# Optimization experiments

Hardware: AMD Instinct MI355X
Metric: run time of the kernel (lower is better)

## Reference

```python
import jax, jax.numpy as jnp
import numpy as np

B, T, DIM = 4, 4096, 1024
HEADS, DIM_HEAD = 16, 64
INNER = HEADS * DIM_HEAD
SCALE = DIM_HEAD ** -0.5


def setup_inputs() -> dict:
    key = jax.random.key(0)
    k1, k2, k3, k4 = jax.random.split(key, 4)
    x = jax.random.normal(k1, (B, T, DIM), dtype=jnp.float32)
    mask = jax.random.bernoulli(k2, 0.2, (B, T))  # True = padding
    W_qkv = jax.random.normal(k3, (DIM, 3 * INNER), dtype=jnp.float32) * (DIM ** -0.5)
    W_out = jax.random.normal(k4, (INNER, DIM), dtype=jnp.float32) * (INNER ** -0.5)
    b_out = jnp.zeros((DIM,), dtype=jnp.float32)
    return {"x": x, "mask": mask, "W_qkv": W_qkv, "W_out": W_out, "b_out": b_out}


def reference(x, mask, W_qkv, W_out, b_out):
    Bs, Ts, _ = x.shape
    qkv = x @ W_qkv                                       # [B,T,3*inner]
    q, k, v = jnp.split(qkv, 3, axis=-1)
    # [B,T,H,Dh] -> [B,H,T,Dh]
    reshape = lambda t: t.reshape(Bs, Ts, HEADS, DIM_HEAD).transpose(0, 2, 1, 3)
    q, k, v = reshape(q), reshape(k), reshape(v)
    q = q * SCALE
    k = jax.nn.softmax(k, axis=-2)                        # softmax over sequence dim
    # zero out padded positions AFTER softmax (faithful to original)
    k = jnp.where(mask[:, None, :, None], 0.0, k)
    context = jnp.einsum('bhnd,bhne->bhde', k, v)         # [B,H,Dh,Dh]
    out = jnp.einsum('bhnd,bhde->bhne', q, context)       # [B,H,T,Dh]
    out = out.transpose(0, 2, 1, 3).reshape(Bs, Ts, INNER)
    return out @ W_out + b_out                            # dropout: eval mode (identity)
```

## Files before the change

kernel.cpp:

```cpp
#include <hip/hip_runtime.h>
#include <math.h>


typedef __bf16 bf16;
typedef __attribute__((ext_vector_type(4))) float f32x4;
typedef __attribute__((ext_vector_type(8))) __bf16 bf16x8;
typedef __attribute__((ext_vector_type(4))) __bf16 bf16x4;

#define SCALE_ 0.125f

__device__ __forceinline__ void g2l16(const void* g, void* l) {
  __builtin_amdgcn_global_load_lds((const __attribute__((address_space(1))) void*)g,
                                   (__attribute__((address_space(3))) void*)l, 16, 0, 0);
}

__global__ __launch_bounds__(256) void k_cvt(const float* __restrict__ in,
                                             bf16* __restrict__ out, int n4) {
  int i = blockIdx.x * 256 + threadIdx.x;
  if (i >= n4) return;
  f32x4 v = ((const f32x4*)in)[i];
  bf16x4 o;
  o[0] = (bf16)v[0]; o[1] = (bf16)v[1]; o[2] = (bf16)v[2]; o[3] = (bf16)v[3];
  ((bf16x4*)out)[i] = o;
}

__global__ __launch_bounds__(256) void k_trans(const float* __restrict__ W,
                                               bf16* __restrict__ Wt) {
  __shared__ float t[32][33];
  int n0 = blockIdx.x * 32, k0 = blockIdx.y * 32;
  int tx = threadIdx.x & 31, ty = threadIdx.x >> 5;
  #pragma unroll
  for (int s = 0; s < 4; s++) {
    int k = ty + s * 8;
    t[k][tx] = W[(size_t)(k0 + k) * 3072 + 1024 + n0 + tx];
  }
  __syncthreads();
  #pragma unroll
  for (int s = 0; s < 4; s++) {
    int n = ty + s * 8;
    Wt[(size_t)(n0 + n) * 1024 + k0 + tx] = (bf16)t[tx][n];
  }
}

__global__ __launch_bounds__(256) void k_wq(const float* __restrict__ W,
                                            bf16* __restrict__ wqs) {
  int idx = blockIdx.x * 256 + threadIdx.x;
  int i = idx >> 8, d4 = idx & 255;
  f32x4 v = *(const f32x4*)(W + (size_t)i * 3072 + d4 * 4);
  bf16x4 o;
  o[0] = (bf16)(v[0] * SCALE_); o[1] = (bf16)(v[1] * SCALE_);
  o[2] = (bf16)(v[2] * SCALE_); o[3] = (bf16)(v[3] * SCALE_);
  *(bf16x4*)(wqs + (size_t)i * 1024 + d4 * 4) = o;
}

__global__ __launch_bounds__(256) void k_gemm1(const bf16* __restrict__ A,
                                               const bf16* __restrict__ Bt,
                                               bf16* __restrict__ kv) {
  __shared__ __align__(16) bf16 As[128 * 32];
  __shared__ __align__(16) bf16 Bs[128 * 32];
  const int tid = threadIdx.x;
  const int wave = tid >> 6, lane = tid & 63, l16 = lane & 15, quad = lane >> 4;
  const int wm = (wave >> 1) << 6, wn = (wave & 1) << 6;
  const int f = blockIdx.x, xcd = f & 7, w = f >> 3;
  const int row0 = (xcd * 16 + (w >> 4)) << 7;
  const int col0 = (w & 15) << 7;
  f32x4 acc[4][4] = {};
  for (int kt = 0; kt < 1024; kt += 32) {
    #pragma unroll
    for (int it = 0; it < 2; ++it) {
      const int cb = (wave * 2 + it) * 64;
      const int c = cb + lane;
      const int m = c >> 2, k8 = (c & 3) * 8;
      g2l16(A  + (size_t)(row0 + m) * 1024 + kt + k8, As + cb * 8);
      g2l16(Bt + (size_t)(col0 + m) * 1024 + kt + k8, Bs + cb * 8);
    }
    __syncthreads();
    bf16x8 af[4], bfr[4];
    #pragma unroll
    for (int i = 0; i < 4; i++) af[i]  = *(const bf16x8*)(As + (wm + i * 16 + l16) * 32 + quad * 8);
    #pragma unroll
    for (int j = 0; j < 4; j++) bfr[j] = *(const bf16x8*)(Bs + (wn + j * 16 + l16) * 32 + quad * 8);
    #pragma unroll
    for (int i = 0; i < 4; i++)
      #pragma unroll
      for (int j = 0; j < 4; j++)
        acc[i][j] = __builtin_amdgcn_mfma_f32_16x16x32_bf16(af[i], bfr[j], acc[i][j], 0, 0, 0);
    __syncthreads();
  }
  #pragma unroll
  for (int i = 0; i < 4; i++) {
    const int gm0 = row0 + wm + i * 16 + quad * 4;
    #pragma unroll
    for (int j = 0; j < 4; j++) {
      const int gc = col0 + wn + j * 16 + l16;
      #pragma unroll
      for (int r = 0; r < 4; r++)
        kv[(size_t)(gm0 + r) * 2048 + gc] = (bf16)acc[i][j][r];
    }
  }
}

__global__ __launch_bounds__(256) void k_ctx(const bf16* __restrict__ kv,
                                             const int* __restrict__ mask,
                                             float* __restrict__ sumexp,
                                             float* __restrict__ ctx) {
  __shared__ float Lk[64][68];
  __shared__ float Lv[64][68];
  __shared__ float Sst[64][33];
  const int blk = blockIdx.x, tid = threadIdx.x;
  const int wave = tid >> 6, lane = tid & 63;
  const int ns = blk & 7, h = (blk >> 3) & 15, b = blk >> 7;
  const int d0 = (lane & 7) * 8, e0 = (lane >> 3) * 8;
  const int g = tid & 7;
  float acc[8][8] = {};
  float sum8[8] = {};
  const int nbase = ns * 512;
  for (int ch = 0; ch < 8; ++ch) {
    const int n0 = nbase + ch * 64;
    __syncthreads();
    #pragma unroll
    for (int it = 0; it < 2; ++it) {
      const int idx = it * 256 + tid;
      const int row = idx >> 3;
      const int gn = b * 4096 + n0 + row;
      const float m = mask[gn] ? 0.f : 1.f;
      bf16x8 t8 = *(const bf16x8*)(kv + (size_t)gn * 2048 + h * 64 + g * 8);
      float e[8];
      #pragma unroll
      for (int j = 0; j < 8; j++) { e[j] = __expf((float)t8[j]); sum8[j] += e[j]; }
      f32x4 lo, hi;
      lo[0] = e[0] * m; lo[1] = e[1] * m; lo[2] = e[2] * m; lo[3] = e[3] * m;
      hi[0] = e[4] * m; hi[1] = e[5] * m; hi[2] = e[6] * m; hi[3] = e[7] * m;
      *(f32x4*)&Lk[row][g * 8] = lo;
      *(f32x4*)&Lk[row][g * 8 + 4] = hi;
    }
    #pragma unroll
    for (int it = 0; it < 2; ++it) {
      const int idx = it * 256 + tid;
      const int row = idx >> 3;
      const int gn = b * 4096 + n0 + row;
      bf16x8 t8 = *(const bf16x8*)(kv + (size_t)gn * 2048 + 1024 + h * 64 + g * 8);
      f32x4 lo, hi;
      lo[0] = (float)t8[0]; lo[1] = (float)t8[1]; lo[2] = (float)t8[2]; lo[3] = (float)t8[3];
      hi[0] = (float)t8[4]; hi[1] = (float)t8[5]; hi[2] = (float)t8[6]; hi[3] = (float)t8[7];
      *(f32x4*)&Lv[row][g * 8] = lo;
      *(f32x4*)&Lv[row][g * 8 + 4] = hi;
    }
    __syncthreads();
    #pragma unroll 4
    for (int t = 0; t < 16; t++) {
      const int n = (wave << 4) + t;
      f32x4 ka = *(const f32x4*)&Lk[n][d0];
      f32x4 kb = *(const f32x4*)&Lk[n][d0 + 4];
      f32x4 va = *(const f32x4*)&Lv[n][e0];
      f32x4 vb = *(const f32x4*)&Lv[n][e0 + 4];
      float kk[8] = {ka[0], ka[1], ka[2], ka[3], kb[0], kb[1], kb[2], kb[3]};
      float vv[8] = {va[0], va[1], va[2], va[3], vb[0], vb[1], vb[2], vb[3]};
      #pragma unroll
      for (int a = 0; a < 8; a++)
        #pragma unroll
        for (int c = 0; c < 8; c++) acc[a][c] += kk[a] * vv[c];
    }
  }
  __syncthreads();
  float* r0 = &Lk[0][0];
  float* r1 = &Lv[0][0];
  if (wave < 2) {
    float* r = wave ? r1 : r0;
    #pragma unroll
    for (int a = 0; a < 8; a++)
      #pragma unroll
      for (int c = 0; c < 8; c++) r[(d0 + a) * 64 + e0 + c] = acc[a][c];
  }
  {
    const int rg = tid >> 3;
    #pragma unroll
    for (int j = 0; j < 8; j++) Sst[g * 8 + j][rg] = sum8[j];
  }
  __syncthreads();
  if (wave >= 2) {
    float* r = (wave == 3) ? r1 : r0;
    #pragma unroll
    for (int a = 0; a < 8; a++)
      #pragma unroll
      for (int c = 0; c < 8; c++) r[(d0 + a) * 64 + e0 + c] += acc[a][c];
  } else if (tid < 64) {
    float s = 0.f;
    #pragma unroll 8
    for (int rg = 0; rg < 32; rg++) s += Sst[tid][rg];
    atomicAdd(&sumexp[b * 1024 + h * 64 + tid], s);
  }
  __syncthreads();
  float* cbase = ctx + ((size_t)(b * 16 + h) << 12);
  for (int i = tid; i < 4096; i += 256) atomicAdd(cbase + i, r0[i] + r1[i]);
}

__global__ __launch_bounds__(256) void k_m2(const float* __restrict__ ctx,
                                            const float* __restrict__ sumexp,
                                            const float* __restrict__ Wout,
                                            bf16* __restrict__ M2t) {
  __shared__ float Lc[64][64];
  __shared__ float Linv[64];
  const int b = blockIdx.z, h = blockIdx.y, jt = blockIdx.x;
  const int tid = threadIdx.x, dg = tid >> 6, jl = tid & 63;
  const float* cbase = ctx + ((size_t)(b * 16 + h) << 12);
  for (int i = tid; i < 4096; i += 256) (&Lc[0][0])[i] = cbase[i];
  if (tid < 64) Linv[tid] = 1.f / sumexp[b * 1024 + h * 64 + tid];
  __syncthreads();
  float acc[4][16] = {};
  const int j0 = jt * 256 + jl;
  for (int e = 0; e < 64; e++) {
    const float* wrow = Wout + (size_t)(h * 64 + e) * 1024 + j0;
    float w0 = wrow[0], w1 = wrow[64], w2 = wrow[128], w3 = wrow[192];
    #pragma unroll
    for (int dd = 0; dd < 16; dd++) {
      float c = Lc[dg * 16 + dd][e];
      acc[0][dd] += c * w0; acc[1][dd] += c * w1;
      acc[2][dd] += c * w2; acc[3][dd] += c * w3;
    }
  }
  #pragma unroll
  for (int jj = 0; jj < 4; jj++) {
    const size_t jrow = ((size_t)b << 20) + (size_t)(jt * 256 + jl + jj * 64) * 1024 + h * 64 + dg * 16;
    #pragma unroll
    for (int dd = 0; dd < 16; dd++)
      M2t[jrow + dd] = (bf16)(acc[jj][dd] * Linv[dg * 16 + dd]);
  }
}

__global__ __launch_bounds__(256) void k_m3(const bf16* __restrict__ M2t,
                                            const bf16* __restrict__ wqs,
                                            bf16* __restrict__ M3t) {
  __shared__ __align__(16) bf16 As[128 * 32];
  __shared__ __align__(16) bf16 Bs[128 * 32];
  const int tid = threadIdx.x;
  const int wave = tid >> 6, lane = tid & 63, l16 = lane & 15, quad = lane >> 4;
  const int wm = (wave >> 1) << 6, wn = (wave & 1) << 6;
  const int row0 = blockIdx.y << 7, col0 = blockIdx.x << 7;
  const bf16* A  = M2t + ((size_t)blockIdx.z << 20);
  bf16*       C  = M3t + ((size_t)blockIdx.z << 20);
  f32x4 acc[4][4] = {};
  for (int kt = 0; kt < 1024; kt += 32) {
    #pragma unroll
    for (int it = 0; it < 2; ++it) {
      const int cb = (wave * 2 + it) * 64;
      const int c = cb + lane;
      const int m = c >> 2, k8 = (c & 3) * 8;
      g2l16(A   + (size_t)(row0 + m) * 1024 + kt + k8, As + cb * 8);
      g2l16(wqs + (size_t)(col0 + m) * 1024 + kt + k8, Bs + cb * 8);
    }
    __syncthreads();
    bf16x8 af[4], bfr[4];
    #pragma unroll
    for (int i = 0; i < 4; i++) af[i]  = *(const bf16x8*)(As + (wm + i * 16 + l16) * 32 + quad * 8);
    #pragma unroll
    for (int j = 0; j < 4; j++) bfr[j] = *(const bf16x8*)(Bs + (wn + j * 16 + l16) * 32 + quad * 8);
    #pragma unroll
    for (int i = 0; i < 4; i++)
      #pragma unroll
      for (int j = 0; j < 4; j++)
        acc[i][j] = __builtin_amdgcn_mfma_f32_16x16x32_bf16(af[i], bfr[j], acc[i][j], 0, 0, 0);
    __syncthreads();
  }
  #pragma unroll
  for (int i = 0; i < 4; i++) {
    const int gm0 = row0 + wm + i * 16 + quad * 4;
    #pragma unroll
    for (int j = 0; j < 4; j++) {
      const int gc = col0 + wn + j * 16 + l16;
      #pragma unroll
      for (int r = 0; r < 4; r++)
        C[(size_t)(gm0 + r) * 1024 + gc] = (bf16)acc[i][j][r];
    }
  }
}

__global__ __launch_bounds__(256) void k_gemm2(const bf16* __restrict__ A,
                                               const bf16* __restrict__ M3t,
                                               const float* __restrict__ bias,
                                               float* __restrict__ out) {
  __shared__ __align__(16) bf16 As[128 * 32];
  __shared__ __align__(16) bf16 Bs[128 * 32];
  const int tid = threadIdx.x;
  const int wave = tid >> 6, lane = tid & 63, l16 = lane & 15, quad = lane >> 4;
  const int wm = (wave >> 1) << 6, wn = (wave & 1) << 6;
  const int f = blockIdx.x, xcd = f & 7, w = f >> 3;
  const int row0 = (xcd * 16 + (w >> 3)) << 7;
  const int col0 = (w & 7) << 7;
  const bf16* Bt = M3t + ((size_t)(row0 >> 12) << 20);
  f32x4 acc[4][4] = {};
  for (int kt = 0; kt < 1024; kt += 32) {
    #pragma unroll
    for (int it = 0; it < 2; ++it) {
      const int cb = (wave * 2 + it) * 64;
      const int c = cb + lane;
      const int m = c >> 2, k8 = (c & 3) * 8;
      g2l16(A  + (size_t)(row0 + m) * 1024 + kt + k8, As + cb * 8);
      g2l16(Bt + (size_t)(col0 + m) * 1024 + kt + k8, Bs + cb * 8);
    }
    __syncthreads();
    bf16x8 af[4], bfr[4];
    #pragma unroll
    for (int i = 0; i < 4; i++) af[i]  = *(const bf16x8*)(As + (wm + i * 16 + l16) * 32 + quad * 8);
    #pragma unroll
    for (int j = 0; j < 4; j++) bfr[j] = *(const bf16x8*)(Bs + (wn + j * 16 + l16) * 32 + quad * 8);
    #pragma unroll
    for (int i = 0; i < 4; i++)
      #pragma unroll
      for (int j = 0; j < 4; j++)
        acc[i][j] = __builtin_amdgcn_mfma_f32_16x16x32_bf16(af[i], bfr[j], acc[i][j], 0, 0, 0);
    __syncthreads();
  }
  float bj[4];
  #pragma unroll
  for (int j = 0; j < 4; j++) bj[j] = bias[col0 + wn + j * 16 + l16];
  #pragma unroll
  for (int i = 0; i < 4; i++) {
    const int gm0 = row0 + wm + i * 16 + quad * 4;
    #pragma unroll
    for (int j = 0; j < 4; j++) {
      const int gc = col0 + wn + j * 16 + l16;
      #pragma unroll
      for (int r = 0; r < 4; r++)
        out[(size_t)(gm0 + r) * 1024 + gc] = acc[i][j][r] + bj[j];
    }
  }
}

extern "C" void kernel_launch(void* const* d_in, const int* in_sizes, int n_in,
                              void* d_out, int out_size, void* d_ws, size_t ws_size,
                              hipStream_t stream) {
  const float* x    = (const float*)d_in[0];
  const int*   mask = (const int*)d_in[1];
  const float* Wqkv = (const float*)d_in[2];
  const float* Wout = (const float*)d_in[3];
  const float* bout = (const float*)d_in[4];
  float* out = (float*)d_out;
  char* ws = (char*)d_ws;
  bf16*  xb     = (bf16*)(ws);
  bf16*  wt     = (bf16*)(ws + 33554432);
  bf16*  wqs    = (bf16*)(ws + 37748736);
  bf16*  kv     = (bf16*)(ws + 39845888);
  float* sumexp = (float*)(ws + 106954752);
  float* ctx    = (float*)(ws + 106971136);
  bf16*  m2t    = (bf16*)(ws + 108019712);
  bf16*  m3t    = (bf16*)(ws + 116408320);

  hipMemsetAsync(sumexp, 0, 16384 + 1048576, stream);
  k_cvt  <<<16384, 256, 0, stream>>>(x, xb, 4194304);
  k_trans<<<dim3(64, 32), 256, 0, stream>>>(Wqkv, wt);
  k_wq   <<<1024, 256, 0, stream>>>(Wqkv, wqs);
  k_gemm1<<<2048, 256, 0, stream>>>(xb, wt, kv);
  k_ctx  <<<512, 256, 0, stream>>>(kv, mask, sumexp, ctx);
  k_m2   <<<dim3(4, 16, 4), 256, 0, stream>>>(ctx, sumexp, Wout, m2t);
  k_m3   <<<dim3(8, 8, 4), 256, 0, stream>>>(m2t, wqs, m3t);
  k_gemm2<<<1024, 256, 0, stream>>>(xb, m3t, bout, out);
}
```

Baseline: 350.9 us.

## Triple-buffer GEMM K-loop with async LDS prefetch and XOR-swizzled tiles

Replaces the synchronous load-then-compute K loop in the three bf16 MFMA GEMMs with a three-stage LDS ring buffer. Tiles are prefetched two steps ahead through global_load_lds, and vmcnt waits plus raw barriers let global loads overlap MFMA work. An XOR swizzle on the 8-element k-chunks is meant to cut LDS bank conflicts on fragment reads. In exchange, LDS use per block triples and the code depends on hand-counted vmcnt values that must match the number of outstanding loads.

Result: slower. 363.1 us (+3.5%).

```diff
diff --git a/kernel.cpp b/kernel.cpp
--- a/kernel.cpp
+++ b/kernel.cpp
@@ -53,11 +53,67 @@
   *(bf16x4*)(wqs + (size_t)i * 1024 + d4 * 4) = o;
 }
 
+__device__ __forceinline__ void stage_tile(const bf16* __restrict__ A,
+                                           const bf16* __restrict__ Bt,
+                                           int row0, int col0, int kt,
+                                           bf16* as, bf16* bs,
+                                           int wave, int lane) {
+  #pragma unroll
+  for (int it = 0; it < 2; ++it) {
+    const int cb = (wave * 2 + it) * 64;
+    const int c = cb + lane;
+    const int m = c >> 2;
+    const int ks = ((c & 3) ^ (m & 3)) * 8;
+    g2l16(A  + (size_t)(row0 + m) * 1024 + kt + ks, as + cb * 8);
+    g2l16(Bt + (size_t)(col0 + m) * 1024 + kt + ks, bs + cb * 8);
+  }
+}
+
+__device__ __forceinline__ void mfma_step(const bf16* as, const bf16* bs,
+                                          int wm, int wn, int l16, int quad,
+                                          f32x4 acc[4][4]) {
+  bf16x8 af[4], bfr[4];
+  const int sw = quad ^ (l16 & 3);
+  #pragma unroll
+  for (int i = 0; i < 4; i++)
+    af[i]  = *(const bf16x8*)(as + ((wm + i * 16 + l16) * 4 + sw) * 8);
+  #pragma unroll
+  for (int j = 0; j < 4; j++)
+    bfr[j] = *(const bf16x8*)(bs + ((wn + j * 16 + l16) * 4 + sw) * 8);
+  #pragma unroll
+  for (int i = 0; i < 4; i++)
+    #pragma unroll
+    for (int j = 0; j < 4; j++)
+      acc[i][j] = __builtin_amdgcn_mfma_f32_16x16x32_bf16(af[i], bfr[j], acc[i][j], 0, 0, 0);
+}
+
+#define GEMM_KLOOP(A_, B_, row0_, col0_)                                      \
+  stage_tile(A_, B_, row0_, col0_, 0,  As,        Bs,        wave, lane);     \
+  stage_tile(A_, B_, row0_, col0_, 32, As + 4096, Bs + 4096, wave, lane);     \
+  for (int t = 0; t < 30; ++t) {                                             \
+    const int bn = ((t + 2) % 3) * 4096;                                     \
+    stage_tile(A_, B_, row0_, col0_, (t + 2) * 32, As + bn, Bs + bn, wave, lane); \
+    asm volatile("s_waitcnt vmcnt(8)" ::: "memory");                         \
+    __builtin_amdgcn_s_barrier();                                            \
+    const int bc = (t % 3) * 4096;                                           \
+    mfma_step(As + bc, Bs + bc, wm, wn, l16, quad, acc);                     \
+    __builtin_amdgcn_sched_barrier(0);                                       \
+    __builtin_amdgcn_s_barrier();                                            \
+  }                                                                          \
+  asm volatile("s_waitcnt vmcnt(4)" ::: "memory");                           \
+  __builtin_amdgcn_s_barrier();                                              \
+  mfma_step(As + 0 * 4096, Bs + 0 * 4096, wm, wn, l16, quad, acc);           \
+  __builtin_amdgcn_sched_barrier(0);                                         \
+  __builtin_amdgcn_s_barrier();                                              \
+  asm volatile("s_waitcnt vmcnt(0)" ::: "memory");                           \
+  __builtin_amdgcn_s_barrier();                                              \
+  mfma_step(As + 1 * 4096, Bs + 1 * 4096, wm, wn, l16, quad, acc);
+
 __global__ __launch_bounds__(256) void k_gemm1(const bf16* __restrict__ A,
                                                const bf16* __restrict__ Bt,
                                                bf16* __restrict__ kv) {
-  __shared__ __align__(16) bf16 As[128 * 32];
-  __shared__ __align__(16) bf16 Bs[128 * 32];
+  __shared__ __align__(16) bf16 As[3 * 4096];
+  __shared__ __align__(16) bf16 Bs[3 * 4096];
   const int tid = threadIdx.x;
   const int wave = tid >> 6, lane = tid & 63, l16 = lane & 15, quad = lane >> 4;
   const int wm = (wave >> 1) << 6, wn = (wave & 1) << 6;
@@ -65,28 +121,7 @@
   const int row0 = (xcd * 16 + (w >> 4)) << 7;
   const int col0 = (w & 15) << 7;
   f32x4 acc[4][4] = {};
-  for (int kt = 0; kt < 1024; kt += 32) {
-    #pragma unroll
-    for (int it = 0; it < 2; ++it) {
-      const int cb = (wave * 2 + it) * 64;
-      const int c = cb + lane;
-      const int m = c >> 2, k8 = (c & 3) * 8;
-      g2l16(A  + (size_t)(row0 + m) * 1024 + kt + k8, As + cb * 8);
-      g2l16(Bt + (size_t)(col0 + m) * 1024 + kt + k8, Bs + cb * 8);
-    }
-    __syncthreads();
-    bf16x8 af[4], bfr[4];
-    #pragma unroll
-    for (int i = 0; i < 4; i++) af[i]  = *(const bf16x8*)(As + (wm + i * 16 + l16) * 32 + quad * 8);
-    #pragma unroll
-    for (int j = 0; j < 4; j++) bfr[j] = *(const bf16x8*)(Bs + (wn + j * 16 + l16) * 32 + quad * 8);
-    #pragma unroll
-    for (int i = 0; i < 4; i++)
-      #pragma unroll
-      for (int j = 0; j < 4; j++)
-        acc[i][j] = __builtin_amdgcn_mfma_f32_16x16x32_bf16(af[i], bfr[j], acc[i][j], 0, 0, 0);
-    __syncthreads();
-  }
+  GEMM_KLOOP(A, Bt, row0, col0)
   #pragma unroll
   for (int i = 0; i < 4; i++) {
     const int gm0 = row0 + wm + i * 16 + quad * 4;
@@ -231,8 +266,8 @@
 __global__ __launch_bounds__(256) void k_m3(const bf16* __restrict__ M2t,
                                             const bf16* __restrict__ wqs,
                                             bf16* __restrict__ M3t) {
-  __shared__ __align__(16) bf16 As[128 * 32];
-  __shared__ __align__(16) bf16 Bs[128 * 32];
+  __shared__ __align__(16) bf16 As[3 * 4096];
+  __shared__ __align__(16) bf16 Bs[3 * 4096];
   const int tid = threadIdx.x;
   const int wave = tid >> 6, lane = tid & 63, l16 = lane & 15, quad = lane >> 4;
   const int wm = (wave >> 1) << 6, wn = (wave & 1) << 6;
@@ -240,28 +275,7 @@
   const bf16* A  = M2t + ((size_t)blockIdx.z << 20);
   bf16*       C  = M3t + ((size_t)blockIdx.z << 20);
   f32x4 acc[4][4] = {};
-  for (int kt = 0; kt < 1024; kt += 32) {
-    #pragma unroll
-    for (int it = 0; it < 2; ++it) {
-      const int cb = (wave * 2 + it) * 64;
-      const int c = cb + lane;
-      const int m = c >> 2, k8 = (c & 3) * 8;
-      g2l16(A   + (size_t)(row0 + m) * 1024 + kt + k8, As + cb * 8);
-      g2l16(wqs + (size_t)(col0 + m) * 1024 + kt + k8, Bs + cb * 8);
-    }
-    __syncthreads();
-    bf16x8 af[4], bfr[4];
-    #pragma unroll
-    for (int i = 0; i < 4; i++) af[i]  = *(const bf16x8*)(As + (wm + i * 16 + l16) * 32 + quad * 8);
-    #pragma unroll
-    for (int j = 0; j < 4; j++) bfr[j] = *(const bf16x8*)(Bs + (wn + j * 16 + l16) * 32 + quad * 8);
-    #pragma unroll
-    for (int i = 0; i < 4; i++)
-      #pragma unroll
-      for (int j = 0; j < 4; j++)
-        acc[i][j] = __builtin_amdgcn_mfma_f32_16x16x32_bf16(af[i], bfr[j], acc[i][j], 0, 0, 0);
-    __syncthreads();
-  }
+  GEMM_KLOOP(A, wqs, row0, col0)
   #pragma unroll
   for (int i = 0; i < 4; i++) {
     const int gm0 = row0 + wm + i * 16 + quad * 4;
@@ -279,8 +293,8 @@
                                                const bf16* __restrict__ M3t,
                                                const float* __restrict__ bias,
                                                float* __restrict__ out) {
-  __shared__ __align__(16) bf16 As[128 * 32];
-  __shared__ __align__(16) bf16 Bs[128 * 32];
+  __shared__ __align__(16) bf16 As[3 * 4096];
+  __shared__ __align__(16) bf16 Bs[3 * 4096];
   const int tid = threadIdx.x;
   const int wave = tid >> 6, lane = tid & 63, l16 = lane & 15, quad = lane >> 4;
   const int wm = (wave >> 1) << 6, wn = (wave & 1) << 6;
@@ -289,28 +303,7 @@
   const int col0 = (w & 7) << 7;
   const bf16* Bt = M3t + ((size_t)(row0 >> 12) << 20);
   f32x4 acc[4][4] = {};
-  for (int kt = 0; kt < 1024; kt += 32) {
-    #pragma unroll
-    for (int it = 0; it < 2; ++it) {
-      const int cb = (wave * 2 + it) * 64;
-      const int c = cb + lane;
-      const int m = c >> 2, k8 = (c & 3) * 8;
-      g2l16(A  + (size_t)(row0 + m) * 1024 + kt + k8, As + cb * 8);
-      g2l16(Bt + (size_t)(col0 + m) * 1024 + kt + k8, Bs + cb * 8);
-    }
-    __syncthreads();
-    bf16x8 af[4], bfr[4];
-    #pragma unroll
-    for (int i = 0; i < 4; i++) af[i]  = *(const bf16x8*)(As + (wm + i * 16 + l16) * 32 + quad * 8);
-    #pragma unroll
-    for (int j = 0; j < 4; j++) bfr[j] = *(const bf16x8*)(Bs + (wn + j * 16 + l16) * 32 + quad * 8);
-    #pragma unroll
-    for (int i = 0; i < 4; i++)
-      #pragma unroll
-      for (int j = 0; j < 4; j++)
-        acc[i][j] = __builtin_amdgcn_mfma_f32_16x16x32_bf16(af[i], bfr[j], acc[i][j], 0, 0, 0);
-    __syncthreads();
-  }
+  GEMM_KLOOP(A, Bt, row0, col0)
   float bj[4];
   #pragma unroll
   for (int j = 0; j < 4; j++) bj[j] = bias[col0 + wn + j * 16 + l16];
```

## Rewrite both GEMMs with 256x256 tiles and double-buffered swizzled LDS pipeline

Applied to the files above, without the earlier changes.

Replaces the two 128x128 single-buffered GEMM kernels with a shared 256x256-tile core using 512 threads. The core uses 128KB of LDS double-buffered in 32-wide k sub-tiles, with an XOR swizzle to avoid bank conflicts. Global-to-LDS prefetches are interleaved with MFMA phases under explicit vmcnt waits, barriers and s_setprio. The aim is to raise arithmetic intensity per block and hide load latency behind compute. The cost is heavy LDS use (one block per CU) and fewer blocks, which may hurt tail balance.

Result: faster. 326.0 us (-7.1%).

```diff
diff --git a/kernel.cpp b/kernel.cpp
--- a/kernel.cpp
+++ b/kernel.cpp
@@ -53,49 +53,104 @@
   *(bf16x4*)(wqs + (size_t)i * 1024 + d4 * 4) = o;
 }
 
-__global__ __launch_bounds__(256) void k_gemm1(const bf16* __restrict__ A,
-                                               const bf16* __restrict__ Bt,
-                                               bf16* __restrict__ kv) {
-  __shared__ __align__(16) bf16 As[128 * 32];
-  __shared__ __align__(16) bf16 Bs[128 * 32];
+
+__device__ __forceinline__ void stage_unit(const bf16* __restrict__ G, int base_row,
+                                           int kcol, void* ldsBase, int tid) {
+  #pragma unroll
+  for (int r = 0; r < 2; ++r) {
+    const int d  = tid * 16 + r * 8192;
+    const int lb = d ^ (((d >> 7) & 3) << 4);
+    g2l16(G + (size_t)(base_row + (lb >> 6)) * 1024 + kcol + ((lb & 63) >> 1),
+          (char*)ldsBase + d);
+  }
+}
+
+#define VM8() asm volatile("s_waitcnt vmcnt(8)" ::: "memory")
+
+#define PHASE(DB, MH, KS, LOADB, ...)                                         \
+  {                                                                           \
+    const char* Ab_ = Lraw + (DB) * 65536 + (KS) * 16384;                     \
+    _Pragma("unroll") for (int i_ = 0; i_ < 4; ++i_)                          \
+      af[i_] = *(const bf16x8*)(Ab_ + aoff[MH][i_]);                          \
+    if (LOADB) {                                                              \
+      _Pragma("unroll") for (int j_ = 0; j_ < 4; ++j_)                        \
+        bfr[j_] = *(const bf16x8*)(Ab_ + 32768 + boff[j_]);                   \
+    }                                                                         \
+    __VA_ARGS__;                                                              \
+    __builtin_amdgcn_s_barrier();                                             \
+    __builtin_amdgcn_s_setprio(1);                                            \
+    _Pragma("unroll") for (int i_ = 0; i_ < 4; ++i_)                          \
+      _Pragma("unroll") for (int j_ = 0; j_ < 4; ++j_)                        \
+        acc[(MH) * 4 + i_][j_] = __builtin_amdgcn_mfma_f32_16x16x32_bf16(     \
+            af[i_], bfr[j_], acc[(MH) * 4 + i_][j_], 0, 0, 0);                \
+    __builtin_amdgcn_s_setprio(0);                                            \
+    __builtin_amdgcn_s_barrier();                                             \
+  }
+
+__device__ __forceinline__ void gemm256_core(const bf16* __restrict__ A_,
+                                             const bf16* __restrict__ B_,
+                                             int row0, int col0,
+                                             char* Lraw, f32x4 (&acc)[8][4]) {
   const int tid = threadIdx.x;
   const int wave = tid >> 6, lane = tid & 63, l16 = lane & 15, quad = lane >> 4;
-  const int wm = (wave >> 1) << 6, wn = (wave & 1) << 6;
+  const int wr = wave >> 2, wc = wave & 3;
+  int aoff[2][4], boff[4];
+  #pragma unroll
+  for (int mh = 0; mh < 2; ++mh)
+    #pragma unroll
+    for (int i = 0; i < 4; ++i) {
+      const int row = wr * 128 + mh * 64 + i * 16 + l16;
+      aoff[mh][i] = row * 64 + ((quad ^ ((row >> 1) & 3)) << 4);
+    }
+  #pragma unroll
+  for (int j = 0; j < 4; ++j) {
+    const int row = wc * 64 + j * 16 + l16;
+    boff[j] = row * 64 + ((quad ^ ((row >> 1) & 3)) << 4);
+  }
+  bf16x8 af[4], bfr[4];
+  stage_unit(A_, row0, 0,  Lraw + 0,      tid);
+  stage_unit(B_, col0, 0,  Lraw + 32768,  tid);
+  stage_unit(A_, row0, 32, Lraw + 16384,  tid);
+  stage_unit(B_, col0, 32, Lraw + 49152,  tid);
+  stage_unit(A_, row0, 64, Lraw + 65536,  tid);
+  stage_unit(B_, col0, 64, Lraw + 98304,  tid);
+  VM8();
+  __builtin_amdgcn_s_barrier();
+  for (int I = 0; I < 8; ++I) {
+    const int k1 = (2 * I + 1) * 64, k2 = (2 * I + 2) * 64, k3 = (2 * I + 3) * 64;
+    const bool pf = (I < 7);
+    PHASE(0, 0, 0, true,  { stage_unit(A_, row0, k1 + 32, Lraw + 65536 + 16384, tid); })
+    PHASE(0, 1, 0, false, { stage_unit(B_, col0, k1 + 32, Lraw + 65536 + 49152, tid); VM8(); })
+    PHASE(0, 0, 1, true,  { if (pf) stage_unit(A_, row0, k2,      Lraw + 0,     tid); })
+    PHASE(0, 1, 1, false, { if (pf) stage_unit(B_, col0, k2,      Lraw + 32768, tid); VM8(); })
+    PHASE(1, 0, 0, true,  { if (pf) stage_unit(A_, row0, k2 + 32, Lraw + 16384, tid); })
+    PHASE(1, 1, 0, false, { if (pf) stage_unit(B_, col0, k2 + 32, Lraw + 49152, tid); VM8(); })
+    PHASE(1, 0, 1, true,  { if (pf) stage_unit(A_, row0, k3,      Lraw + 65536, tid); })
+    PHASE(1, 1, 1, false, { if (pf) stage_unit(B_, col0, k3,      Lraw + 98304, tid); VM8(); })
+  }
+}
+
+__global__ __launch_bounds__(512, 2) void k_gemm1(const bf16* __restrict__ A,
+                                                  const bf16* __restrict__ Bt,
+                                                  bf16* __restrict__ kv) {
+  __shared__ __align__(16) char Lraw[131072];
   const int f = blockIdx.x, xcd = f & 7, w = f >> 3;
-  const int row0 = (xcd * 16 + (w >> 4)) << 7;
-  const int col0 = (w & 15) << 7;
-  f32x4 acc[4][4] = {};
-  for (int kt = 0; kt < 1024; kt += 32) {
-    #pragma unroll
-    for (int it = 0; it < 2; ++it) {
-      const int cb = (wave * 2 + it) * 64;
-      const int c = cb + lane;
-      const int m = c >> 2, k8 = (c & 3) * 8;
-      g2l16(A  + (size_t)(row0 + m) * 1024 + kt + k8, As + cb * 8);
-      g2l16(Bt + (size_t)(col0 + m) * 1024 + kt + k8, Bs + cb * 8);
-    }
-    __syncthreads();
-    bf16x8 af[4], bfr[4];
-    #pragma unroll
-    for (int i = 0; i < 4; i++) af[i]  = *(const bf16x8*)(As + (wm + i * 16 + l16) * 32 + quad * 8);
-    #pragma unroll
-    for (int j = 0; j < 4; j++) bfr[j] = *(const bf16x8*)(Bs + (wn + j * 16 + l16) * 32 + quad * 8);
-    #pragma unroll
-    for (int i = 0; i < 4; i++)
-      #pragma unroll
-      for (int j = 0; j < 4; j++)
-        acc[i][j] = __builtin_amdgcn_mfma_f32_16x16x32_bf16(af[i], bfr[j], acc[i][j], 0, 0, 0);
-    __syncthreads();
-  }
-  #pragma unroll
-  for (int i = 0; i < 4; i++) {
-    const int gm0 = row0 + wm + i * 16 + quad * 4;
-    #pragma unroll
-    for (int j = 0; j < 4; j++) {
-      const int gc = col0 + wn + j * 16 + l16;
-      #pragma unroll
-      for (int r = 0; r < 4; r++)
-        kv[(size_t)(gm0 + r) * 2048 + gc] = (bf16)acc[i][j][r];
+  const int row0 = (xcd * 8 + (w >> 3)) << 8;
+  const int col0 = (w & 7) << 8;
+  f32x4 acc[8][4] = {};
+  gemm256_core(A, Bt, row0, col0, Lraw, acc);
+  const int tid = threadIdx.x;
+  const int wave = tid >> 6, lane = tid & 63, l16 = lane & 15, quad = lane >> 4;
+  const int wr = wave >> 2, wc = wave & 3;
+  #pragma unroll
+  for (int ai = 0; ai < 8; ++ai) {
+    const int gm0 = row0 + wr * 128 + ai * 16 + quad * 4;
+    #pragma unroll
+    for (int j = 0; j < 4; ++j) {
+      const int gc = col0 + wc * 64 + j * 16 + l16;
+      #pragma unroll
+      for (int r = 0; r < 4; ++r)
+        kv[(size_t)(gm0 + r) * 2048 + gc] = (bf16)acc[ai][j][r];
     }
   }
 }
@@ -275,54 +330,32 @@
   }
 }
 
-__global__ __launch_bounds__(256) void k_gemm2(const bf16* __restrict__ A,
-                                               const bf16* __restrict__ M3t,
-                                               const float* __restrict__ bias,
-                                               float* __restrict__ out) {
-  __shared__ __align__(16) bf16 As[128 * 32];
-  __shared__ __align__(16) bf16 Bs[128 * 32];
+__global__ __launch_bounds__(512, 2) void k_gemm2(const bf16* __restrict__ A,
+                                                  const bf16* __restrict__ M3t,
+                                                  const float* __restrict__ bias,
+                                                  float* __restrict__ out) {
+  __shared__ __align__(16) char Lraw[131072];
+  const int f = blockIdx.x, xcd = f & 7, w = f >> 3;
+  const int row0 = (xcd * 8 + (w >> 2)) << 8;
+  const int col0 = (w & 3) << 8;
+  const bf16* Bt = M3t + ((size_t)(row0 >> 12) << 20);
+  f32x4 acc[8][4] = {};
+  gemm256_core(A, Bt, row0, col0, Lraw, acc);
   const int tid = threadIdx.x;
   const int wave = tid >> 6, lane = tid & 63, l16 = lane & 15, quad = lane >> 4;
-  const int wm = (wave >> 1) << 6, wn = (wave & 1) << 6;
-  const int f = blockIdx.x, xcd = f & 7, w = f >> 3;
-  const int row0 = (xcd * 16 + (w >> 3)) << 7;
-  const int col0 = (w & 7) << 7;
-  const bf16* Bt = M3t + ((size_t)(row0 >> 12) << 20);
-  f32x4 acc[4][4] = {};
-  for (int kt = 0; kt < 1024; kt += 32) {
-    #pragma unroll
-    for (int it = 0; it < 2; ++it) {
-      const int cb = (wave * 2 + it) * 64;
-      const int c = cb + lane;
-      const int m = c >> 2, k8 = (c & 3) * 8;
-      g2l16(A  + (size_t)(row0 + m) * 1024 + kt + k8, As + cb * 8);
-      g2l16(Bt + (size_t)(col0 + m) * 1024 + kt + k8, Bs + cb * 8);
-    }
-    __syncthreads();
-    bf16x8 af[4], bfr[4];
-    #pragma unroll
-    for (int i = 0; i < 4; i++) af[i]  = *(const bf16x8*)(As + (wm + i * 16 + l16) * 32 + quad * 8);
-    #pragma unroll
-    for (int j = 0; j < 4; j++) bfr[j] = *(const bf16x8*)(Bs + (wn + j * 16 + l16) * 32 + quad * 8);
-    #pragma unroll
-    for (int i = 0; i < 4; i++)
-      #pragma unroll
-      for (int j = 0; j < 4; j++)
-        acc[i][j] = __builtin_amdgcn_mfma_f32_16x16x32_bf16(af[i], bfr[j], acc[i][j], 0, 0, 0);
-    __syncthreads();
-  }
+  const int wr = wave >> 2, wc = wave & 3;
   float bj[4];
   #pragma unroll
-  for (int j = 0; j < 4; j++) bj[j] = bias[col0 + wn + j * 16 + l16];
-  #pragma unroll
-  for (int i = 0; i < 4; i++) {
-    const int gm0 = row0 + wm + i * 16 + quad * 4;
-    #pragma unroll
-    for (int j = 0; j < 4; j++) {
-      const int gc = col0 + wn + j * 16 + l16;
-      #pragma unroll
-      for (int r = 0; r < 4; r++)
-        out[(size_t)(gm0 + r) * 1024 + gc] = acc[i][j][r] + bj[j];
+  for (int j = 0; j < 4; j++) bj[j] = bias[col0 + wc * 64 + j * 16 + l16];
+  #pragma unroll
+  for (int ai = 0; ai < 8; ++ai) {
+    const int gm0 = row0 + wr * 128 + ai * 16 + quad * 4;
+    #pragma unroll
+    for (int j = 0; j < 4; ++j) {
+      const int gc = col0 + wc * 64 + j * 16 + l16;
+      #pragma unroll
+      for (int r = 0; r < 4; ++r)
+        out[(size_t)(gm0 + r) * 1024 + gc] = acc[ai][j][r] + bj[j];
     }
   }
 }
@@ -350,9 +383,9 @@
   k_cvt  <<<16384, 256, 0, stream>>>(x, xb, 4194304);
   k_trans<<<dim3(64, 32), 256, 0, stream>>>(Wqkv, wt);
   k_wq   <<<1024, 256, 0, stream>>>(Wqkv, wqs);
-  k_gemm1<<<2048, 256, 0, stream>>>(xb, wt, kv);
+  k_gemm1<<<512, 512, 0, stream>>>(xb, wt, kv);
   k_ctx  <<<512, 256, 0, stream>>>(kv, mask, sumexp, ctx);
   k_m2   <<<dim3(4, 16, 4), 256, 0, stream>>>(ctx, sumexp, Wout, m2t);
   k_m3   <<<dim3(8, 8, 4), 256, 0, stream>>>(m2t, wqs, m3t);
-  k_gemm2<<<1024, 256, 0, stream>>>(xb, m3t, bout, out);
-}
+  k_gemm2<<<256, 512, 0, stream>>>(xb, m3t, bout, out);
+}
```
